# Optimization experiments

Measured on AMD Instinct MI355X. Metric: run time of the kernel, lower is better.

Reference implementation:

```python
import jax, jax.numpy as jnp
import numpy as np

DT_MIN, DT_MAX = 1e-3, 0.1
BSZ, SEQ, DM, DS = 8, 2048, 1024, 16


def setup_inputs() -> dict:
    key = jax.random.key(0)
    ks = jax.random.split(key, 8)
    x = jax.random.normal(ks[0], (BSZ, SEQ, DM), jnp.float32)
    a_log = jax.random.normal(ks[1], (DM, DS), jnp.float32) * -0.5
    b = jax.random.normal(ks[2], (DM, DS), jnp.float32) * 0.02
    c = jax.random.normal(ks[3], (DM, DS), jnp.float32) * 0.02
    dt_w = jax.random.normal(ks[4], (DM, DM), jnp.float32) * (1.0 / np.sqrt(DM))
    dt_b = jnp.zeros((DM,), jnp.float32)
    conv_w = jax.random.normal(ks[5], (DM, 1, 3), jnp.float32) * (1.0 / np.sqrt(3.0))
    conv_b = jnp.zeros((DM,), jnp.float32)
    return {"x": x, "a_log": a_log, "b": b, "c": c, "dt_w": dt_w, "dt_b": dt_b, "conv_w": conv_w, "conv_b": conv_b}


def _depthwise_conv(x, conv_w, conv_b):
    # x: (B,N,C) -> (B,C,N) depthwise conv k=3, pad=1 -> (B,N,C)
    xc = jnp.transpose(x, (0, 2, 1))
    y = jax.lax.conv_general_dilated(
        xc, conv_w, window_strides=(1,), padding=[(1, 1)],
        feature_group_count=xc.shape[1],
        dimension_numbers=("NCH", "OIH", "NCH"))
    y = y + conv_b[None, :, None]
    return jnp.transpose(y, (0, 2, 1))


def reference(x, a_log, b, c, dt_w, dt_b, conv_w, conv_b):
    Bn, N, C = x.shape
    D = a_log.shape[1]
    xf = _depthwise_conv(x, conv_w, conv_b)                      # (B,N,C)
    dt = jax.nn.sigmoid(xf @ dt_w.T + dt_b) * (DT_MAX - DT_MIN) + DT_MIN  # (B,N,C)
    A = -jax.nn.softplus(a_log)                                   # (C,D)

    def step(s, inp):
        xt, dtt = inp                                             # each (B,C)
        expA = jnp.exp(dtt[..., None] * A)                        # (B,C,D)
        s = expA * s + (dtt * xt)[..., None] * b                  # (B,C,D)
        y = jnp.einsum("bcd,cd->bc", s, c)
        return s, y

    s0 = jnp.zeros((Bn, C, D), x.dtype)
    xs = (jnp.transpose(xf, (1, 0, 2)), jnp.transpose(dt, (1, 0, 2)))
    _, ys = jax.lax.scan(step, s0, xs)                            # (N,B,C)
    return jnp.transpose(ys, (1, 0, 2))                           # (B,N,C)
```

## Files before the change

kernel.cpp:

```cpp
#include <hip/hip_runtime.h>
#include <stdint.h>

#define BSZ 8
#define SEQ 2048
#define DM 1024
#define DS 16
#define MROWS (BSZ * SEQ)
#define CHK 64
#define CLEN (SEQ / CHK)
#define LOG2E 1.4426950408889634f

typedef __bf16 bf16x8 __attribute__((ext_vector_type(8)));
typedef float f32x4 __attribute__((ext_vector_type(4)));

union F4 { float4 v; float f[4]; };

__device__ __forceinline__ uint16_t f2bf(float f) {
  uint32_t u = __float_as_uint(f);
  u += 0x7FFFu + ((u >> 16) & 1u);
  return (uint16_t)(u >> 16);
}

__device__ __forceinline__ void async_cp16(const void* g, void* l) {
  __builtin_amdgcn_global_load_lds(
      (const __attribute__((address_space(1))) uint32_t*)(uintptr_t)g,
      (__attribute__((address_space(3))) uint32_t*)(uint32_t)(uintptr_t)l,
      16, 0, 0);
}

__global__ __launch_bounds__(256) void wprep_kernel(
    const float* __restrict__ w, uint16_t* __restrict__ wb) {
  int t = blockIdx.x * 256 + threadIdx.x;
  F4 u; u.v = *(const float4*)(w + (size_t)t * 4);
  uint32_t lo = f2bf(u.f[0]) | ((uint32_t)f2bf(u.f[1]) << 16);
  uint32_t hi = f2bf(u.f[2]) | ((uint32_t)f2bf(u.f[3]) << 16);
  *(uint2*)(wb + (size_t)t * 4) = make_uint2(lo, hi);
}

__global__ __launch_bounds__(256) void aprep_kernel(
    const float* __restrict__ a_log, const float* __restrict__ bm,
    const float* __restrict__ cm, float* __restrict__ A2c,
    float* __restrict__ A2t, float* __restrict__ cb2) {
  int e = blockIdx.x * 256 + threadIdx.x;
  float a = a_log[e];
  float A2 = -log1pf(__expf(a)) * LOG2E;
  A2c[e] = A2;
  cb2[e] = bm[e] * cm[e];
  int c = e >> 4, d = e & 15;
  int j = d >> 2, i = d & 3;
  A2t[((size_t)j * DM + c) * 4 + i] = A2;
}

__global__ __launch_bounds__(256) void conv_kernel(
    const float* __restrict__ x, const float* __restrict__ cw,
    const float* __restrict__ cb, uint16_t* __restrict__ xf) {
  int t = blockIdx.x * 256 + threadIdx.x;
  int cg = t & (DM / 4 - 1);
  int bn = t >> 8;
  int n = bn & (SEQ - 1);
  int c0 = cg * 4;
  const float* row = x + (size_t)bn * DM + c0;
  F4 xm, xc, xp;
  xm.v = make_float4(0.f, 0.f, 0.f, 0.f);
  xp.v = make_float4(0.f, 0.f, 0.f, 0.f);
  xc.v = *(const float4*)row;
  if (n > 0)       xm.v = *(const float4*)(row - DM);
  if (n < SEQ - 1) xp.v = *(const float4*)(row + DM);
  uint16_t o[4];
#pragma unroll
  for (int j = 0; j < 4; ++j) {
    int c = c0 + j;
    float v = cw[c * 3 + 0] * xm.f[j] + cw[c * 3 + 1] * xc.f[j] +
              cw[c * 3 + 2] * xp.f[j] + cb[c];
    o[j] = f2bf(v);
  }
  uint32_t lo = o[0] | ((uint32_t)o[1] << 16);
  uint32_t hi = o[2] | ((uint32_t)o[3] << 16);
  *(uint2*)(xf + (size_t)bn * DM + c0) = make_uint2(lo, hi);
}

__global__ __launch_bounds__(256) void gemm_kernel(
    const uint16_t* __restrict__ A,
    const uint16_t* __restrict__ B,
    const float* __restrict__ bias,
    float* __restrict__ dt) {
  __shared__ __align__(16) uint16_t As[128 * 64];
  __shared__ __align__(16) uint16_t Bs[128 * 64];
  const int tid = threadIdx.x;
  const int w = tid >> 6;
  const int L = tid & 63;
  const int wm = w & 1, wn = w >> 1;
  const int lane15 = L & 15, q = L >> 4;
  const int m0 = blockIdx.y * 128;
  const int n0 = blockIdx.x * 128;
  const int lr = L >> 3;
  const int lc = (L & 7) * 8;

  f32x4 acc[4][4] = {};

  for (int kt = 0; kt < DM; kt += 64) {
#pragma unroll
    for (int r = 0; r < 4; ++r) {
      int R = (r * 4 + w) * 8;
      async_cp16(A + (size_t)(m0 + R + lr) * DM + kt + lc, &As[R * 64]);
    }
#pragma unroll
    for (int r = 0; r < 4; ++r) {
      int R = (r * 4 + w) * 8;
      async_cp16(B + (size_t)(n0 + R + lr) * DM + kt + lc, &Bs[R * 64]);
    }
    __syncthreads();
#pragma unroll
    for (int ks = 0; ks < 64; ks += 32) {
      bf16x8 af[4], bfr[4];
#pragma unroll
      for (int mi = 0; mi < 4; ++mi)
        af[mi] = *(const bf16x8*)(As + (wm * 64 + mi * 16 + lane15) * 64 + ks + q * 8);
#pragma unroll
      for (int ni = 0; ni < 4; ++ni)
        bfr[ni] = *(const bf16x8*)(Bs + (wn * 64 + ni * 16 + lane15) * 64 + ks + q * 8);
#pragma unroll
      for (int mi = 0; mi < 4; ++mi)
#pragma unroll
        for (int ni = 0; ni < 4; ++ni)
          acc[mi][ni] = __builtin_amdgcn_mfma_f32_16x16x32_bf16(
              af[mi], bfr[ni], acc[mi][ni], 0, 0, 0);
    }
    __syncthreads();
  }

#pragma unroll
  for (int ni = 0; ni < 4; ++ni) {
    int col = n0 + wn * 64 + ni * 16 + lane15;
    float db = bias[col];
#pragma unroll
    for (int mi = 0; mi < 4; ++mi) {
      int rowb = m0 + wm * 64 + mi * 16 + q * 4;
#pragma unroll
      for (int r = 0; r < 4; ++r) {
        float z = acc[mi][ni][r] + db;
        float s = 0.099f / (1.f + __expf(-z)) + 0.001f;
        dt[(size_t)(rowb + r) * DM + col] = s;
      }
    }
  }
}


__global__ __launch_bounds__(256) void scan_part1(
    const float* __restrict__ x, const float* __restrict__ dt,
    const float* __restrict__ A2c, const float* __restrict__ cw,
    const float* __restrict__ cb, float* __restrict__ F,
    float* __restrict__ Sdt) {
  const int c = blockIdx.x * 256 + threadIdx.x;
  const int k = blockIdx.y;
  const int b = blockIdx.z;
  const int n0 = k * CLEN;

  float A2[DS], s[DS];
#pragma unroll
  for (int j = 0; j < 4; ++j) {
    F4 ua; ua.v = *(const float4*)(A2c + (size_t)c * DS + j * 4);
#pragma unroll
    for (int i = 0; i < 4; ++i) {
      A2[j * 4 + i] = ua.f[i];
      s[j * 4 + i] = 0.f;
    }
  }
  const float w0 = cw[c * 3 + 0], w1 = cw[c * 3 + 1], w2 = cw[c * 3 + 2];
  const float cbv = cb[c];

  const float* xp = x + (size_t)b * SEQ * DM + c;
  const float* dp = dt + (size_t)b * SEQ * DM + c;

  float xm1 = (n0 > 0) ? xp[(size_t)(n0 - 1) * DM] : 0.f;
  float x0 = xp[(size_t)n0 * DM];
  float x1 = xp[(size_t)(n0 + 1) * DM];
  float dcur = dp[(size_t)n0 * DM];
  float sdt = 0.f;

  for (int t = 0; t < CLEN; ++t) {
    const int n = n0 + t;
    float xnext = 0.f, dnext = 0.f;
    if (n + 2 < SEQ) xnext = xp[(size_t)(n + 2) * DM];
    if (t + 1 < CLEN) dnext = dp[(size_t)(n + 1) * DM];
    float xf = w0 * xm1 + w1 * x0 + w2 * x1 + cbv;
    float u = dcur * xf;
    sdt += dcur;
#pragma unroll
    for (int d = 0; d < DS; ++d) {
      float e = __builtin_amdgcn_exp2f(dcur * A2[d]);
      s[d] = fmaf(e, s[d], u);
    }
    xm1 = x0; x0 = x1; x1 = xnext; dcur = dnext;
  }

  const size_t kk = (size_t)b * CHK + k;
#pragma unroll
  for (int j = 0; j < 4; ++j) {
    F4 fo;
#pragma unroll
    for (int i = 0; i < 4; ++i) fo.f[i] = s[j * 4 + i];
    *(float4*)(F + ((kk * 4 + j) * DM + c) * 4) = fo.v;
  }
  Sdt[kk * DM + c] = sdt;
}

__global__ __launch_bounds__(256) void scan_combine(
    float* __restrict__ F, const float* __restrict__ Sdt,
    const float* __restrict__ A2t) {
  const int t = blockIdx.x * 256 + threadIdx.x;
  const int b = blockIdx.y;
  const int c = (t >> 2) & (DM - 1);
  const float A2 = A2t[t];
  const size_t stride = (size_t)DM * DS;
  const size_t base = (size_t)b * CHK * stride + t;
  const size_t sbase = (size_t)b * CHK * DM + c;
  float carry = 0.f;
#pragma unroll 4
  for (int k = 0; k < CHK; ++k) {
    const size_t idx = base + (size_t)k * stride;
    float f = F[idx];
    float p = __builtin_amdgcn_exp2f(A2 * Sdt[sbase + (size_t)k * DM]);
    F[idx] = carry;
    carry = fmaf(p, carry, f);
  }
}

__global__ __launch_bounds__(256) void scan_part3(
    const float* __restrict__ x, const float* __restrict__ dt,
    const float* __restrict__ A2c, const float* __restrict__ cb2m,
    const float* __restrict__ cw, const float* __restrict__ cb,
    const float* __restrict__ Sin, float* __restrict__ out) {
  const int c = blockIdx.x * 256 + threadIdx.x;
  const int k = blockIdx.y;
  const int b = blockIdx.z;
  const int n0 = k * CLEN;

  float A2[DS], cb2[DS], s[DS];
  const size_t kk = (size_t)b * CHK + k;
#pragma unroll
  for (int j = 0; j < 4; ++j) {
    F4 ua, uc, us;
    ua.v = *(const float4*)(A2c + (size_t)c * DS + j * 4);
    uc.v = *(const float4*)(cb2m + (size_t)c * DS + j * 4);
    us.v = *(const float4*)(Sin + ((kk * 4 + j) * DM + c) * 4);
#pragma unroll
    for (int i = 0; i < 4; ++i) {
      A2[j * 4 + i] = ua.f[i];
      cb2[j * 4 + i] = uc.f[i];
      s[j * 4 + i] = us.f[i];
    }
  }
  const float w0 = cw[c * 3 + 0], w1 = cw[c * 3 + 1], w2 = cw[c * 3 + 2];
  const float cbv = cb[c];

  const float* xp = x + (size_t)b * SEQ * DM + c;
  const float* dp = dt + (size_t)b * SEQ * DM + c;
  float* op = out + (size_t)b * SEQ * DM + c;

  float xm1 = (n0 > 0) ? xp[(size_t)(n0 - 1) * DM] : 0.f;
  float x0 = xp[(size_t)n0 * DM];
  float x1 = xp[(size_t)(n0 + 1) * DM];
  float dcur = dp[(size_t)n0 * DM];

  for (int t = 0; t < CLEN; ++t) {
    const int n = n0 + t;
    float xnext = 0.f, dnext = 0.f;
    if (n + 2 < SEQ) xnext = xp[(size_t)(n + 2) * DM];
    if (t + 1 < CLEN) dnext = dp[(size_t)(n + 1) * DM];
    float xf = w0 * xm1 + w1 * x0 + w2 * x1 + cbv;
    float u = dcur * xf;
    float y0 = 0.f, y1 = 0.f;
#pragma unroll
    for (int d = 0; d < DS; d += 2) {
      float e0 = __builtin_amdgcn_exp2f(dcur * A2[d]);
      float e1 = __builtin_amdgcn_exp2f(dcur * A2[d + 1]);
      s[d] = fmaf(e0, s[d], u);
      s[d + 1] = fmaf(e1, s[d + 1], u);
      y0 = fmaf(cb2[d], s[d], y0);
      y1 = fmaf(cb2[d + 1], s[d + 1], y1);
    }
    op[(size_t)n * DM] = y0 + y1;
    xm1 = x0; x0 = x1; x1 = xnext; dcur = dnext;
  }
}

extern "C" void kernel_launch(void* const* d_in, const int* in_sizes, int n_in,
                              void* d_out, int out_size, void* d_ws, size_t ws_size,
                              hipStream_t stream) {
  const float* x     = (const float*)d_in[0];
  const float* a_log = (const float*)d_in[1];
  const float* bm    = (const float*)d_in[2];
  const float* cm    = (const float*)d_in[3];
  const float* dt_w  = (const float*)d_in[4];
  const float* dt_b  = (const float*)d_in[5];
  const float* cw    = (const float*)d_in[6];
  const float* cb    = (const float*)d_in[7];
  float* out = (float*)d_out;

  char* ws = (char*)d_ws;
  uint16_t* xf_bf = (uint16_t*)ws;
  uint16_t* w_bf  = (uint16_t*)(ws + (size_t)MROWS * DM * 2);
  float* dt   = (float*)(ws + (size_t)MROWS * DM * 2 + (size_t)DM * DM * 2);
  float* Fbuf = dt + (size_t)MROWS * DM;
  float* Sdt  = Fbuf + (size_t)BSZ * CHK * DM * DS;
  float* A2c  = Sdt + (size_t)BSZ * CHK * DM;
  float* A2t  = A2c + (size_t)DM * DS;
  float* cb2  = A2t + (size_t)DM * DS;

  hipLaunchKernelGGL(wprep_kernel, dim3(DM * DM / 1024), dim3(256), 0, stream,
                     dt_w, w_bf);
  hipLaunchKernelGGL(aprep_kernel, dim3(DM * DS / 256), dim3(256), 0, stream,
                     a_log, bm, cm, A2c, A2t, cb2);
  hipLaunchKernelGGL(conv_kernel, dim3(MROWS * DM / 1024), dim3(256), 0, stream,
                     x, cw, cb, xf_bf);
  hipLaunchKernelGGL(gemm_kernel, dim3(DM / 128, MROWS / 128), dim3(256), 0,
                     stream, xf_bf, w_bf, dt_b, dt);
  hipLaunchKernelGGL(scan_part1, dim3(DM / 256, CHK, BSZ), dim3(256), 0, stream,
                     x, dt, A2c, cw, cb, Fbuf, Sdt);
  hipLaunchKernelGGL(scan_combine, dim3(DM * DS / 256, BSZ), dim3(256), 0,
                     stream, Fbuf, Sdt, A2t);
  hipLaunchKernelGGL(scan_part3, dim3(DM / 256, CHK, BSZ), dim3(256), 0, stream,
                     x, dt, A2c, cb2, cw, cb, Fbuf, out);
}
```

Baseline: 310.0 us.

## Pack dt and dt*x as fp16 pairs in GEMM epilogue; swizzle LDS tiles

The GEMM epilogue now reads the bf16 conv output, computes u = dt*xf, and stores (u, dt) packed as two fp16 values in one 32-bit word. Both scan kernels read this single stream instead of re-reading x, recomputing the conv, and loading fp32 dt, which cuts their global traffic roughly in half. The GEMM also XOR-swizzles its LDS layout to reduce bank conflicts on the bf16x8 fragment loads. The cost is lower precision for dt and u (fp16, with xf already rounded to bf16), plus an extra scattered read of A in the epilogue.

```diff
diff --git a/kernel.cpp b/kernel.cpp
--- a/kernel.cpp
+++ b/kernel.cpp
@@ -19,6 +19,19 @@
   uint32_t u = __float_as_uint(f);
   u += 0x7FFFu + ((u >> 16) & 1u);
   return (uint16_t)(u >> 16);
+}
+
+__device__ __forceinline__ uint32_t pack_h2(float a, float b) {
+  _Float16 ha = (_Float16)a, hb = (_Float16)b;
+  uint16_t ua = __builtin_bit_cast(uint16_t, ha);
+  uint16_t ub = __builtin_bit_cast(uint16_t, hb);
+  return (uint32_t)ua | ((uint32_t)ub << 16);
+}
+__device__ __forceinline__ float unpack_lo(uint32_t v) {
+  return (float)__builtin_bit_cast(_Float16, (uint16_t)(v & 0xffffu));
+}
+__device__ __forceinline__ float unpack_hi(uint32_t v) {
+  return (float)__builtin_bit_cast(_Float16, (uint16_t)(v >> 16));
 }
 
 __device__ __forceinline__ void async_cp16(const void* g, void* l) {
@@ -83,7 +96,7 @@
     const uint16_t* __restrict__ A,
     const uint16_t* __restrict__ B,
     const float* __restrict__ bias,
-    float* __restrict__ dt) {
+    uint32_t* __restrict__ ud) {
   __shared__ __align__(16) uint16_t As[128 * 64];
   __shared__ __align__(16) uint16_t Bs[128 * 64];
   const int tid = threadIdx.x;
@@ -94,7 +107,8 @@
   const int m0 = blockIdx.y * 128;
   const int n0 = blockIdx.x * 128;
   const int lr = L >> 3;
-  const int lc = (L & 7) * 8;
+  const int lc = (((L & 7) ^ lr)) * 8;
+  const int r7 = lane15 & 7;
 
   f32x4 acc[4][4] = {};
 
@@ -113,12 +127,15 @@
 #pragma unroll
     for (int ks = 0; ks < 64; ks += 32) {
       bf16x8 af[4], bfr[4];
+      const int jbase = ks >> 3;
 #pragma unroll
       for (int mi = 0; mi < 4; ++mi)
-        af[mi] = *(const bf16x8*)(As + (wm * 64 + mi * 16 + lane15) * 64 + ks + q * 8);
+        af[mi] = *(const bf16x8*)(As + (wm * 64 + mi * 16 + lane15) * 64 +
+                                  (((jbase + q) ^ r7) << 3));
 #pragma unroll
       for (int ni = 0; ni < 4; ++ni)
-        bfr[ni] = *(const bf16x8*)(Bs + (wn * 64 + ni * 16 + lane15) * 64 + ks + q * 8);
+        bfr[ni] = *(const bf16x8*)(Bs + (wn * 64 + ni * 16 + lane15) * 64 +
+                                   (((jbase + q) ^ r7) << 3));
 #pragma unroll
       for (int mi = 0; mi < 4; ++mi)
 #pragma unroll
@@ -138,9 +155,11 @@
       int rowb = m0 + wm * 64 + mi * 16 + q * 4;
 #pragma unroll
       for (int r = 0; r < 4; ++r) {
+        size_t idx = (size_t)(rowb + r) * DM + col;
         float z = acc[mi][ni][r] + db;
-        float s = 0.099f / (1.f + __expf(-z)) + 0.001f;
-        dt[(size_t)(rowb + r) * DM + col] = s;
+        float dtv = 0.099f / (1.f + __expf(-z)) + 0.001f;
+        float xfv = __uint_as_float((uint32_t)A[idx] << 16);
+        ud[idx] = pack_h2(dtv * xfv, dtv);
       }
     }
   }
@@ -148,10 +167,8 @@
 
 
 __global__ __launch_bounds__(256) void scan_part1(
-    const float* __restrict__ x, const float* __restrict__ dt,
-    const float* __restrict__ A2c, const float* __restrict__ cw,
-    const float* __restrict__ cb, float* __restrict__ F,
-    float* __restrict__ Sdt) {
+    const uint32_t* __restrict__ ud, const float* __restrict__ A2c,
+    float* __restrict__ F, float* __restrict__ Sdt) {
   const int c = blockIdx.x * 256 + threadIdx.x;
   const int k = blockIdx.y;
   const int b = blockIdx.z;
@@ -167,32 +184,24 @@
       s[j * 4 + i] = 0.f;
     }
   }
-  const float w0 = cw[c * 3 + 0], w1 = cw[c * 3 + 1], w2 = cw[c * 3 + 2];
-  const float cbv = cb[c];
-
-  const float* xp = x + (size_t)b * SEQ * DM + c;
-  const float* dp = dt + (size_t)b * SEQ * DM + c;
-
-  float xm1 = (n0 > 0) ? xp[(size_t)(n0 - 1) * DM] : 0.f;
-  float x0 = xp[(size_t)n0 * DM];
-  float x1 = xp[(size_t)(n0 + 1) * DM];
-  float dcur = dp[(size_t)n0 * DM];
+
+  const uint32_t* up = ud + ((size_t)b * SEQ + n0) * DM + c;
+  uint32_t c0 = up[0];
+  uint32_t c1 = up[DM];
   float sdt = 0.f;
 
   for (int t = 0; t < CLEN; ++t) {
-    const int n = n0 + t;
-    float xnext = 0.f, dnext = 0.f;
-    if (n + 2 < SEQ) xnext = xp[(size_t)(n + 2) * DM];
-    if (t + 1 < CLEN) dnext = dp[(size_t)(n + 1) * DM];
-    float xf = w0 * xm1 + w1 * x0 + w2 * x1 + cbv;
-    float u = dcur * xf;
-    sdt += dcur;
+    uint32_t c2 = 0;
+    if (t + 2 < CLEN) c2 = up[(size_t)(t + 2) * DM];
+    float uv = unpack_lo(c0);
+    float dtv = unpack_hi(c0);
+    sdt += dtv;
 #pragma unroll
     for (int d = 0; d < DS; ++d) {
-      float e = __builtin_amdgcn_exp2f(dcur * A2[d]);
-      s[d] = fmaf(e, s[d], u);
-    }
-    xm1 = x0; x0 = x1; x1 = xnext; dcur = dnext;
+      float e = __builtin_amdgcn_exp2f(dtv * A2[d]);
+      s[d] = fmaf(e, s[d], uv);
+    }
+    c0 = c1; c1 = c2;
   }
 
   const size_t kk = (size_t)b * CHK + k;
@@ -228,10 +237,9 @@
 }
 
 __global__ __launch_bounds__(256) void scan_part3(
-    const float* __restrict__ x, const float* __restrict__ dt,
-    const float* __restrict__ A2c, const float* __restrict__ cb2m,
-    const float* __restrict__ cw, const float* __restrict__ cb,
-    const float* __restrict__ Sin, float* __restrict__ out) {
+    const uint32_t* __restrict__ ud, const float* __restrict__ A2c,
+    const float* __restrict__ cb2m, const float* __restrict__ Sin,
+    float* __restrict__ out) {
   const int c = blockIdx.x * 256 + threadIdx.x;
   const int k = blockIdx.y;
   const int b = blockIdx.z;
@@ -252,37 +260,29 @@
       s[j * 4 + i] = us.f[i];
     }
   }
-  const float w0 = cw[c * 3 + 0], w1 = cw[c * 3 + 1], w2 = cw[c * 3 + 2];
-  const float cbv = cb[c];
-
-  const float* xp = x + (size_t)b * SEQ * DM + c;
-  const float* dp = dt + (size_t)b * SEQ * DM + c;
-  float* op = out + (size_t)b * SEQ * DM + c;
-
-  float xm1 = (n0 > 0) ? xp[(size_t)(n0 - 1) * DM] : 0.f;
-  float x0 = xp[(size_t)n0 * DM];
-  float x1 = xp[(size_t)(n0 + 1) * DM];
-  float dcur = dp[(size_t)n0 * DM];
+
+  const uint32_t* up = ud + ((size_t)b * SEQ + n0) * DM + c;
+  float* op = out + ((size_t)b * SEQ + n0) * DM + c;
+  uint32_t c0 = up[0];
+  uint32_t c1 = up[DM];
 
   for (int t = 0; t < CLEN; ++t) {
-    const int n = n0 + t;
-    float xnext = 0.f, dnext = 0.f;
-    if (n + 2 < SEQ) xnext = xp[(size_t)(n + 2) * DM];
-    if (t + 1 < CLEN) dnext = dp[(size_t)(n + 1) * DM];
-    float xf = w0 * xm1 + w1 * x0 + w2 * x1 + cbv;
-    float u = dcur * xf;
+    uint32_t c2 = 0;
+    if (t + 2 < CLEN) c2 = up[(size_t)(t + 2) * DM];
+    float uv = unpack_lo(c0);
+    float dtv = unpack_hi(c0);
     float y0 = 0.f, y1 = 0.f;
 #pragma unroll
     for (int d = 0; d < DS; d += 2) {
-      float e0 = __builtin_amdgcn_exp2f(dcur * A2[d]);
-      float e1 = __builtin_amdgcn_exp2f(dcur * A2[d + 1]);
-      s[d] = fmaf(e0, s[d], u);
-      s[d + 1] = fmaf(e1, s[d + 1], u);
+      float e0 = __builtin_amdgcn_exp2f(dtv * A2[d]);
+      float e1 = __builtin_amdgcn_exp2f(dtv * A2[d + 1]);
+      s[d] = fmaf(e0, s[d], uv);
+      s[d + 1] = fmaf(e1, s[d + 1], uv);
       y0 = fmaf(cb2[d], s[d], y0);
       y1 = fmaf(cb2[d + 1], s[d + 1], y1);
     }
-    op[(size_t)n * DM] = y0 + y1;
-    xm1 = x0; x0 = x1; x1 = xnext; dcur = dnext;
+    op[(size_t)t * DM] = y0 + y1;
+    c0 = c1; c1 = c2;
   }
 }
 
@@ -302,8 +302,8 @@
   char* ws = (char*)d_ws;
   uint16_t* xf_bf = (uint16_t*)ws;
   uint16_t* w_bf  = (uint16_t*)(ws + (size_t)MROWS * DM * 2);
-  float* dt   = (float*)(ws + (size_t)MROWS * DM * 2 + (size_t)DM * DM * 2);
-  float* Fbuf = dt + (size_t)MROWS * DM;
+  uint32_t* ud = (uint32_t*)(ws + (size_t)MROWS * DM * 2 + (size_t)DM * DM * 2);
+  float* Fbuf = (float*)(ud + (size_t)MROWS * DM);
   float* Sdt  = Fbuf + (size_t)BSZ * CHK * DM * DS;
   float* A2c  = Sdt + (size_t)BSZ * CHK * DM;
   float* A2t  = A2c + (size_t)DM * DS;
@@ -316,11 +316,11 @@
   hipLaunchKernelGGL(conv_kernel, dim3(MROWS * DM / 1024), dim3(256), 0, stream,
                      x, cw, cb, xf_bf);
   hipLaunchKernelGGL(gemm_kernel, dim3(DM / 128, MROWS / 128), dim3(256), 0,
-                     stream, xf_bf, w_bf, dt_b, dt);
+                     stream, xf_bf, w_bf, dt_b, ud);
   hipLaunchKernelGGL(scan_part1, dim3(DM / 256, CHK, BSZ), dim3(256), 0, stream,
-                     x, dt, A2c, cw, cb, Fbuf, Sdt);
+                     ud, A2c, Fbuf, Sdt);
   hipLaunchKernelGGL(scan_combine, dim3(DM * DS / 256, BSZ), dim3(256), 0,
                      stream, Fbuf, Sdt, A2t);
   hipLaunchKernelGGL(scan_part3, dim3(DM / 256, CHK, BSZ), dim3(256), 0, stream,
-                     x, dt, A2c, cb2, cw, cb, Fbuf, out);
-}
+                     ud, A2c, cb2, Fbuf, out);
+}
```

New measurement: 297.4 us. 4.1% less time.
